# Kernel tuning notes

Hardware: AMD Instinct MI355X
Metric: run time of the kernel (lower is better)

The kernel has to match this reference:

```python
import jax, jax.numpy as jnp
import numpy as np

B, L = 4, 2048
D_MODEL, D_STATE, D_CONV, N_BLOCKS = 128, 16, 8, 6
EXPAND = 2
D_INNER = EXPAND * D_MODEL          # 256
DT_RANK = (D_MODEL + 15) // 16      # 8
CONV_K = 7                          # pre_conv kernel


def setup_inputs() -> dict:
    key = jax.random.key(0)
    ks = jax.random.split(key, 10)
    f = lambda k, s: jax.random.normal(k, s, jnp.float32)
    sc = 0.02
    A_init = jnp.broadcast_to(
        jnp.log(jnp.arange(1, D_STATE + 1, dtype=jnp.float32)),
        (N_BLOCKS, D_INNER, D_STATE)) + 0.0
    return {
        "x": f(ks[0], (B, L, 1)),
        "pre_conv_w": f(ks[1], (D_MODEL, 1, CONV_K)) * sc,
        "pre_conv_b": jnp.zeros((D_MODEL,), jnp.float32),
        "ln_w": jnp.ones((N_BLOCKS, D_MODEL), jnp.float32),
        "ln_b": jnp.zeros((N_BLOCKS, D_MODEL), jnp.float32),
        "W_in": f(ks[2], (N_BLOCKS, 2 * D_INNER, D_MODEL)) * sc,
        "conv_w": f(ks[3], (N_BLOCKS, D_INNER, 1, D_CONV)) * sc,  # depthwise OIH
        "conv_b": jnp.zeros((N_BLOCKS, D_INNER), jnp.float32),
        "W_x": f(ks[4], (N_BLOCKS, DT_RANK + 2 * D_STATE, D_INNER)) * sc,
        "W_dt": f(ks[5], (N_BLOCKS, D_INNER, DT_RANK)) * sc,
        "b_dt": jnp.full((N_BLOCKS, D_INNER), -4.6, jnp.float32),  # softplus ~ 0.01
        "A_log": A_init,
        "D_skip": jnp.ones((N_BLOCKS, D_INNER), jnp.float32),
        "W_out": f(ks[6], (N_BLOCKS, D_MODEL, D_INNER)) * sc,
        "out_w": f(ks[7], (1, D_MODEL)) * sc,
        "out_b": jnp.zeros((1,), jnp.float32),
    }


def _layernorm(x, w, b, eps=1e-5):
    m = jnp.mean(x, axis=-1, keepdims=True)
    v = jnp.mean(jnp.square(x - m), axis=-1, keepdims=True)
    return (x - m) * jax.lax.rsqrt(v + eps) * w + b


def _mamba(x, W_in, cw, cb, W_x, W_dt, b_dt, A_log, D_skip, W_out):
    # x: (B, L, D_MODEL)
    xz = jnp.einsum('bld,ed->ble', x, W_in)            # (B,L,2E)
    xi, z = jnp.split(xz, 2, axis=-1)
    # depthwise causal conv over time
    xc = jax.lax.conv_general_dilated(
        xi.transpose(0, 2, 1), cw, window_strides=(1,),
        padding=[(D_CONV - 1, 0)],
        dimension_numbers=('NCH', 'OIH', 'NCH'),
        feature_group_count=D_INNER) + cb[None, :, None]
    xc = jax.nn.silu(xc).transpose(0, 2, 1)            # (B,L,E)
    dbl = jnp.einsum('ble,re->blr', xc, W_x)
    dt = dbl[..., :DT_RANK]
    Bm = dbl[..., DT_RANK:DT_RANK + D_STATE]           # (B,L,N)
    Cm = dbl[..., DT_RANK + D_STATE:]                  # (B,L,N)
    delta = jax.nn.softplus(jnp.einsum('blr,er->ble', dt, W_dt) + b_dt)
    A = -jnp.exp(A_log)                                # (E,N)

    def step(h, inp):
        d, b, c, u = inp                               # (B,E),(B,N),(B,N),(B,E)
        h = h * jnp.exp(d[..., None] * A) + (d * u)[..., None] * b[:, None, :]
        return h, jnp.einsum('ben,bn->be', h, c)

    h0 = jnp.zeros((x.shape[0], D_INNER, D_STATE), x.dtype)
    xs = (delta.transpose(1, 0, 2), Bm.transpose(1, 0, 2),
          Cm.transpose(1, 0, 2), xc.transpose(1, 0, 2))
    _, ys = jax.lax.scan(step, h0, xs)                 # ys: (L,B,E)
    y = ys.transpose(1, 0, 2) + D_skip * xc
    y = y * jax.nn.silu(z)
    return jnp.einsum('ble,de->bld', y, W_out)


def reference(x, pre_conv_w, pre_conv_b, ln_w, ln_b, W_in, conv_w, conv_b,
              W_x, W_dt, b_dt, A_log, D_skip, W_out, out_w, out_b):
    # pre_conv (1 -> d_model), SAME padding, then exact GELU
    h = jax.lax.conv_general_dilated(
        x.transpose(0, 2, 1), pre_conv_w, window_strides=(1,),
        padding=[(CONV_K // 2, CONV_K // 2)],
        dimension_numbers=('NCH', 'OIH', 'NCH')) + pre_conv_b[None, :, None]
    h = jax.nn.gelu(h, approximate=False).transpose(0, 2, 1)  # (B,L,D)

    def block(carry, p):
        lw, lb, Wi, cw, cb, Wx, Wdt, bdt, Alog, Dsk, Wo = p
        y = _mamba(_layernorm(carry, lw, lb), Wi, cw, cb, Wx, Wdt, bdt, Alog, Dsk, Wo)
        return carry + y, None                         # dropout is identity (eval)

    h, _ = jax.lax.scan(block, h, (ln_w, ln_b, W_in, conv_w, conv_b,
                                   W_x, W_dt, b_dt, A_log, D_skip, W_out))
    return (jnp.einsum('bld,od->blo', h, out_w) + out_b)[..., 0]  # (B,L)
```

## Files before the change

### kernel.cpp

```cpp
#include <hip/hip_runtime.h>
#include <hip/hip_bf16.h>
#include <hip/hip_cooperative_groups.h>
#include <math.h>

namespace cg = cooperative_groups;

#define BB 4
#define LL 2048
#define DM 128
#define DI 256
#define DS 16
#define DTR 8
#define NB 6
#define KPRE 7
#define KC 8
#define NC 128
#define CT 16
#define NCHUNK (BB*NC)
#define BL (BB*LL)
#define SU 4

typedef __attribute__((ext_vector_type(8))) short short8v;
typedef __attribute__((ext_vector_type(4))) short short4v;
typedef __attribute__((ext_vector_type(4))) float f32x4;

__device__ __forceinline__ void store_bf16x4(__hip_bfloat16* p, float a, float b, float c, float d) {
    __hip_bfloat16 t[4] = {__float2bfloat16(a), __float2bfloat16(b),
                           __float2bfloat16(c), __float2bfloat16(d)};
    *(short4v*)p = *(const short4v*)t;
}
__device__ __forceinline__ float4 load_bf16x4(const __hip_bfloat16* p) {
    short4v raw = *(const short4v*)p;
    const __hip_bfloat16* t = (const __hip_bfloat16*)&raw;
    return make_float4(__bfloat162float(t[0]), __bfloat162float(t[1]),
                       __bfloat162float(t[2]), __bfloat162float(t[3]));
}


__device__ __forceinline__ void dev_preconv(int idx,
    const float* __restrict__ x, const float* __restrict__ w, const float* __restrict__ bias,
    float* __restrict__ h, const float* __restrict__ Wi, const float* __restrict__ Wo,
    __hip_bfloat16* __restrict__ wi, __hip_bfloat16* __restrict__ wo) {
    int d = idx & (DM - 1);
    int l = (idx >> 7) & (LL - 1);
    int b = idx >> 18;
    float acc = bias[d];
#pragma unroll
    for (int k = 0; k < KPRE; ++k) {
        int pos = l + k - 3;
        float xv = (pos >= 0 && pos < LL) ? x[b * LL + pos] : 0.f;
        acc = fmaf(xv, w[d * KPRE + k], acc);
    }
    h[idx] = 0.5f * acc * (1.f + erff(acc * 0.70710678118654752f));
    if (idx < NB * 2 * DI * DM) wi[idx] = __float2bfloat16(Wi[idx]);
    if (idx < NB * DM * DI)     wo[idx] = __float2bfloat16(Wo[idx]);
}

__device__ __forceinline__ void dev_ln_gemm1(int v, int wave, int lane,
    const float* __restrict__ h, const float* __restrict__ lw, const float* __restrict__ lb,
    const __hip_bfloat16* __restrict__ W, float* __restrict__ xz,
    __hip_bfloat16* As) {
    int tileM = v >> 2, tileN = v & 3;
    int mBase = tileM * 64, nBase = tileN * 128;
    for (int it = 0; it < 16; ++it) {
        int row = wave * 16 + it;
        int t = mBase + row;
        float v0 = h[t * DM + lane];
        float v1 = h[t * DM + lane + 64];
        float s = v0 + v1;
#pragma unroll
        for (int off = 32; off; off >>= 1) s += __shfl_xor(s, off);
        float mean = s * (1.f / 128.f);
        float d0 = v0 - mean, d1 = v1 - mean;
        float q = d0 * d0 + d1 * d1;
#pragma unroll
        for (int off = 32; off; off >>= 1) q += __shfl_xor(q, off);
        float rstd = rsqrtf(q * (1.f / 128.f) + 1e-5f);
        int sw = (row & 7) << 3;
        As[row * 128 + (lane ^ sw)]        = __float2bfloat16(d0 * rstd * lw[lane] + lb[lane]);
        As[row * 128 + ((lane + 64) ^ sw)] = __float2bfloat16(d1 * rstd * lw[lane + 64] + lb[lane + 64]);
    }
    __syncthreads();
    int r  = lane & 15;
    int kh = lane >> 4;
    f32x4 acc[4][2] = {};
    for (int k0 = 0; k0 < DM; k0 += 32) {
        short8v af[4], bf[2];
#pragma unroll
        for (int i = 0; i < 4; ++i) {
            int row = i * 16 + r;
            int cbk = (k0 >> 3) + kh;
            af[i] = *(const short8v*)&As[row * 128 + ((cbk ^ (row & 7)) << 3)];
        }
#pragma unroll
        for (int j = 0; j < 2; ++j)
            bf[j] = *(const short8v*)&W[(size_t)(nBase + wave * 32 + j * 16 + r) * DM + k0 + kh * 8];
#pragma unroll
        for (int i = 0; i < 4; ++i)
#pragma unroll
            for (int j = 0; j < 2; ++j)
                acc[i][j] = __builtin_amdgcn_mfma_f32_16x16x32_bf16(af[i], bf[j], acc[i][j], 0, 0, 0);
    }
#pragma unroll
    for (int i = 0; i < 4; ++i)
#pragma unroll
        for (int j = 0; j < 2; ++j)
#pragma unroll
            for (int rg = 0; rg < 4; ++rg) {
                size_t off = (size_t)(mBase + i * 16 + kh * 4 + rg) * (2 * DI)
                           + nBase + wave * 32 + j * 16 + r;
                xz[off] = acc[i][j][rg];
            }
    __syncthreads();
}

__device__ __forceinline__ void dev_fusedA(int chunk, int tid,
    const float* __restrict__ xz, const float* __restrict__ cw, const float* __restrict__ cbs,
    const float* __restrict__ Wx, const float* __restrict__ Wdt, const float* __restrict__ bdt,
    const float* __restrict__ A_log,
    __hip_bfloat16* __restrict__ P, __hip_bfloat16* __restrict__ hend,
    float (*xc_s)[DI], float (*dl_s)[DI], float (*bc_s)[32]) {
    int c = chunk & (NC - 1);
    int b = chunk >> 7;
    int wave = tid >> 6, lane = tid & 63;
    for (int i = 0; i < 4; ++i) {
        int lt = wave * 4 + i;
        int tl = c * CT + lt;
        float xv[4];
        for (int j = 0; j < 4; ++j) {
            int e = lane + 64 * j;
            float4 c0 = *(const float4*)&cw[e * KC];
            float4 c1 = *(const float4*)&cw[e * KC + 4];
            float wts[8] = {c0.x, c0.y, c0.z, c0.w, c1.x, c1.y, c1.z, c1.w};
            float acc = cbs[e];
#pragma unroll
            for (int k = 0; k < KC; ++k) {
                int pos = tl + k - (KC - 1);
                float v = (pos >= 0) ? xz[((size_t)(b * LL + pos) << 9) + e] : 0.f;
                acc = fmaf(v, wts[k], acc);
            }
            xv[j] = acc / (1.f + __expf(-acc));
            xc_s[lt][e] = xv[j];
        }
        float dt8[8];
        float bcv = 0.f;
#pragma unroll
        for (int o = 0; o < 40; ++o) {
            const float* w = &Wx[o * DI];
            float s = xv[0] * w[lane];
            s = fmaf(xv[1], w[lane + 64], s);
            s = fmaf(xv[2], w[lane + 128], s);
            s = fmaf(xv[3], w[lane + 192], s);
#pragma unroll
            for (int off = 32; off; off >>= 1) s += __shfl_xor(s, off);
            if (o < 8) dt8[o] = s;
            else if (lane == o - 8) bcv = s;
        }
        if (lane < 32) bc_s[lt][lane] = bcv;
        for (int j = 0; j < 4; ++j) {
            int e = lane + 64 * j;
            float s = bdt[e];
#pragma unroll
            for (int r = 0; r < 8; ++r) s = fmaf(dt8[r], Wdt[e * 8 + r], s);
            dl_s[lt][e] = fmaxf(s, 0.f) + log1pf(__expf(-fabsf(s)));
        }
    }
    __syncthreads();
    int e = tid;
    float d16[CT], u16[CT];
#pragma unroll
    for (int l = 0; l < CT; ++l) { d16[l] = dl_s[l][e]; u16[l] = xc_s[l][e]; }
    for (int ng = 0; ng < 4; ++ng) {
        float4 al = *(const float4*)&A_log[e * DS + 4 * ng];
        float Aen[4] = {-__expf(al.x), -__expf(al.y), -__expf(al.z), -__expf(al.w)};
        float hh[4] = {}, Pl[4] = {1.f, 1.f, 1.f, 1.f};
#pragma unroll
        for (int l = 0; l < CT; ++l) {
            float du = d16[l] * u16[l];
            float4 bm = *(const float4*)&bc_s[l][4 * ng];
            float a0 = __expf(d16[l] * Aen[0]);
            float a1 = __expf(d16[l] * Aen[1]);
            float a2 = __expf(d16[l] * Aen[2]);
            float a3 = __expf(d16[l] * Aen[3]);
            hh[0] = fmaf(hh[0], a0, du * bm.x);
            hh[1] = fmaf(hh[1], a1, du * bm.y);
            hh[2] = fmaf(hh[2], a2, du * bm.z);
            hh[3] = fmaf(hh[3], a3, du * bm.w);
            Pl[0] *= a0; Pl[1] *= a1; Pl[2] *= a2; Pl[3] *= a3;
        }
        size_t oidx = (((size_t)(b * NC + c)) * DI + e) * DS + 4 * ng;
        store_bf16x4(&P[oidx], Pl[0], Pl[1], Pl[2], Pl[3]);
        store_bf16x4(&hend[oidx], hh[0], hh[1], hh[2], hh[3]);
    }
}

__device__ __forceinline__ void dev_carry(int gtid,
    const __hip_bfloat16* __restrict__ P, const __hip_bfloat16* __restrict__ hend,
    __hip_bfloat16* __restrict__ hin) {
    int n = gtid & 15;
    int e = (gtid >> 4) & 255;
    int b = gtid >> 12;
    const size_t cs = (size_t)DI * DS;
    size_t idx0 = (((size_t)(b * NC)) * DI + e) * DS + n;
    float carry = 0.f;
    for (int c0 = 0; c0 < NC; c0 += 8) {
        float p[8], he[8];
#pragma unroll
        for (int j = 0; j < 8; ++j) {
            size_t idx = idx0 + (size_t)(c0 + j) * cs;
            p[j]  = __bfloat162float(P[idx]);
            he[j] = __bfloat162float(hend[idx]);
        }
#pragma unroll
        for (int j = 0; j < 8; ++j) {
            hin[idx0 + (size_t)(c0 + j) * cs] = __float2bfloat16(carry);
            carry = fmaf(p[j], carry, he[j]);
        }
    }
}

__device__ __forceinline__ void dev_fusedB(int chunk, int tid,
    const float* __restrict__ A_log, const __hip_bfloat16* __restrict__ hin,
    const float* __restrict__ xz, const float* __restrict__ Dsk,
    const __hip_bfloat16* __restrict__ Wo, float* __restrict__ hout,
    const float (*xc_s)[DI], const float (*dl_s)[DI], const float (*bc_s)[32],
    __hip_bfloat16 (*y_s)[DI + 8]) {
    int c = chunk & (NC - 1);
    int b = chunk >> 7;
    int base = b * LL + c * CT;
    int e = tid;
    float d16[CT], u16[CT], yacc[CT];
    float dsk = Dsk[e];
#pragma unroll
    for (int l = 0; l < CT; ++l) {
        d16[l] = dl_s[l][e];
        u16[l] = xc_s[l][e];
        yacc[l] = dsk * u16[l];
    }
    for (int ng = 0; ng < 4; ++ng) {
        float4 al = *(const float4*)&A_log[e * DS + 4 * ng];
        float Aen[4] = {-__expf(al.x), -__expf(al.y), -__expf(al.z), -__expf(al.w)};
        float4 h4 = load_bf16x4(&hin[(((size_t)(b * NC + c)) * DI + e) * DS + 4 * ng]);
        float hh[4] = {h4.x, h4.y, h4.z, h4.w};
#pragma unroll
        for (int l = 0; l < CT; ++l) {
            float du = d16[l] * u16[l];
            float4 bm = *(const float4*)&bc_s[l][4 * ng];
            float4 cm = *(const float4*)&bc_s[l][16 + 4 * ng];
            float a0 = __expf(d16[l] * Aen[0]);
            float a1 = __expf(d16[l] * Aen[1]);
            float a2 = __expf(d16[l] * Aen[2]);
            float a3 = __expf(d16[l] * Aen[3]);
            hh[0] = fmaf(hh[0], a0, du * bm.x);
            hh[1] = fmaf(hh[1], a1, du * bm.y);
            hh[2] = fmaf(hh[2], a2, du * bm.z);
            hh[3] = fmaf(hh[3], a3, du * bm.w);
            float p = hh[0] * cm.x;
            p = fmaf(hh[1], cm.y, p);
            p = fmaf(hh[2], cm.z, p);
            p = fmaf(hh[3], cm.w, p);
            yacc[l] += p;
        }
    }
#pragma unroll
    for (int l = 0; l < CT; ++l) {
        float z = xz[((size_t)(base + l) << 9) + DI + e];
        y_s[l][e] = __float2bfloat16(yacc[l] * (z / (1.f + __expf(-z))));
    }
    __syncthreads();
    int wave = tid >> 6, lane = tid & 63;
    int r  = lane & 15;
    int kh = lane >> 4;
    f32x4 acc[2] = {};
    for (int k0 = 0; k0 < DI; k0 += 32) {
        short8v af = *(const short8v*)&y_s[r][k0 + kh * 8];
        short8v bf[2];
#pragma unroll
        for (int j = 0; j < 2; ++j)
            bf[j] = *(const short8v*)&Wo[(size_t)(wave * 32 + j * 16 + r) * DI + k0 + kh * 8];
#pragma unroll
        for (int j = 0; j < 2; ++j)
            acc[j] = __builtin_amdgcn_mfma_f32_16x16x32_bf16(af, bf[j], acc[j], 0, 0, 0);
    }
    __syncthreads();
#pragma unroll
    for (int j = 0; j < 2; ++j)
#pragma unroll
        for (int rg = 0; rg < 4; ++rg) {
            size_t off = (size_t)(base + kh * 4 + rg) * DM + wave * 32 + j * 16 + r;
            hout[off] += acc[j][rg];
        }
}

__device__ __forceinline__ void dev_out(int t, int lane,
    const float* __restrict__ h, const float* __restrict__ ow, const float* __restrict__ ob,
    float* __restrict__ out) {
    float s = h[t * DM + lane] * ow[lane] + h[t * DM + lane + 64] * ow[lane + 64];
#pragma unroll
    for (int off = 32; off; off >>= 1) s += __shfl_xor(s, off);
    if (lane == 0) out[t] = s + ob[0];
}


__device__ __forceinline__ void dev_conv_wx(int t, int lane,
    const float* __restrict__ xz, const float* __restrict__ cw, const float* __restrict__ cbs,
    const float* __restrict__ Wx, const float* __restrict__ Wdt, const float* __restrict__ bdt,
    float* __restrict__ xc, float* __restrict__ BC, float* __restrict__ delta) {
    int tl = t & (LL - 1);
    int b = t >> 11;
    float xv[4];
#pragma unroll
    for (int j = 0; j < 4; ++j) {
        int e = lane + 64 * j;
        float4 cw0 = *(const float4*)&cw[e * KC];
        float4 cw1 = *(const float4*)&cw[e * KC + 4];
        float wts[8] = {cw0.x, cw0.y, cw0.z, cw0.w, cw1.x, cw1.y, cw1.z, cw1.w};
        float acc = cbs[e];
#pragma unroll
        for (int k = 0; k < KC; ++k) {
            int pos = tl + k - (KC - 1);
            float v = (pos >= 0) ? xz[((size_t)(b * LL + pos) << 9) + e] : 0.f;
            acc = fmaf(v, wts[k], acc);
        }
        xv[j] = acc / (1.f + __expf(-acc));
        xc[((size_t)t << 8) + e] = xv[j];
    }
    float dt[8];
    float bcv = 0.f;
#pragma unroll
    for (int o = 0; o < 40; ++o) {
        const float* w = &Wx[o * DI];
        float s = xv[0] * w[lane];
        s = fmaf(xv[1], w[lane + 64], s);
        s = fmaf(xv[2], w[lane + 128], s);
        s = fmaf(xv[3], w[lane + 192], s);
#pragma unroll
        for (int off = 32; off; off >>= 1) s += __shfl_xor(s, off);
        if (o < 8) dt[o] = s;
        else if (lane == o - 8) bcv = s;
    }
    if (lane < 32) BC[((size_t)t << 5) + lane] = bcv;
#pragma unroll
    for (int j = 0; j < 4; ++j) {
        int e = lane + 64 * j;
        float s = bdt[e];
#pragma unroll
        for (int r = 0; r < 8; ++r) s = fmaf(dt[r], Wdt[e * 8 + r], s);
        delta[((size_t)t << 8) + e] = fmaxf(s, 0.f) + log1pf(__expf(-fabsf(s)));
    }
}

__device__ __forceinline__ void dev_scan1(int blk, int tid,
    const float* __restrict__ delta, const float* __restrict__ xc, const float* __restrict__ BC,
    const float* __restrict__ A_log,
    __hip_bfloat16* __restrict__ P, __hip_bfloat16* __restrict__ hend) {
    int eg = blk & 3;
    int c = (blk >> 2) & (NC - 1);
    int b = blk >> 9;
    int e = eg * 64 + (tid >> 2);
    int ng = tid & 3;
    float4 al = *(const float4*)&A_log[e * DS + 4 * ng];
    float Aen[4] = {-__expf(al.x), -__expf(al.y), -__expf(al.z), -__expf(al.w)};
    float h[4] = {}, Pl[4] = {1.f, 1.f, 1.f, 1.f};
    int base = b * LL + c * CT;
    const float* dp = delta + (size_t)base * DI + e;
    const float* up = xc + (size_t)base * DI + e;
    const float* bp = BC + (size_t)base * 32 + 4 * ng;
    for (int l0 = 0; l0 < CT; l0 += SU) {
        float d[SU], u[SU];
        float4 bm[SU];
#pragma unroll
        for (int j = 0; j < SU; ++j) {
            d[j]  = dp[(l0 + j) * DI];
            u[j]  = up[(l0 + j) * DI];
            bm[j] = *(const float4*)&bp[(l0 + j) * 32];
        }
#pragma unroll
        for (int j = 0; j < SU; ++j) {
            float du = d[j] * u[j];
            float a0 = __expf(d[j] * Aen[0]);
            float a1 = __expf(d[j] * Aen[1]);
            float a2 = __expf(d[j] * Aen[2]);
            float a3 = __expf(d[j] * Aen[3]);
            h[0] = fmaf(h[0], a0, du * bm[j].x);
            h[1] = fmaf(h[1], a1, du * bm[j].y);
            h[2] = fmaf(h[2], a2, du * bm[j].z);
            h[3] = fmaf(h[3], a3, du * bm[j].w);
            Pl[0] *= a0; Pl[1] *= a1; Pl[2] *= a2; Pl[3] *= a3;
        }
    }
    size_t oidx = (((size_t)(b * NC + c)) * DI + e) * DS + 4 * ng;
    store_bf16x4(&P[oidx], Pl[0], Pl[1], Pl[2], Pl[3]);
    store_bf16x4(&hend[oidx], h[0], h[1], h[2], h[3]);
}

__device__ __forceinline__ void dev_scan3(int blk, int tid,
    const float* __restrict__ delta, const float* __restrict__ xc, const float* __restrict__ BC,
    const float* __restrict__ A_log, const __hip_bfloat16* __restrict__ hin,
    const float* __restrict__ xz,
    const float* __restrict__ Dsk, __hip_bfloat16* __restrict__ y) {
    int eg = blk & 3;
    int c = (blk >> 2) & (NC - 1);
    int b = blk >> 9;
    int e = eg * 64 + (tid >> 2);
    int ng = tid & 3;
    float4 al = *(const float4*)&A_log[e * DS + 4 * ng];
    float Aen[4] = {-__expf(al.x), -__expf(al.y), -__expf(al.z), -__expf(al.w)};
    float dsk = Dsk[e];
    float4 h4 = load_bf16x4(&hin[(((size_t)(b * NC + c)) * DI + e) * DS + 4 * ng]);
    float h[4] = {h4.x, h4.y, h4.z, h4.w};
    int base = b * LL + c * CT;
    const float* dp = delta + (size_t)base * DI + e;
    const float* up = xc + (size_t)base * DI + e;
    const float* bp = BC + (size_t)base * 32 + 4 * ng;
    const float* zp = xz + ((size_t)base << 9) + DI + e;
    __hip_bfloat16* yp = y + (size_t)base * DI + e;
    for (int l0 = 0; l0 < CT; l0 += SU) {
        float d[SU], u[SU], zv[SU];
        float4 bm[SU], cm[SU];
#pragma unroll
        for (int j = 0; j < SU; ++j) {
            d[j]  = dp[(l0 + j) * DI];
            u[j]  = up[(l0 + j) * DI];
            bm[j] = *(const float4*)&bp[(l0 + j) * 32];
            cm[j] = *(const float4*)&bp[(l0 + j) * 32 + 16];
            zv[j] = zp[(size_t)(l0 + j) << 9];
        }
#pragma unroll
        for (int j = 0; j < SU; ++j) {
            float du = d[j] * u[j];
            float a0 = __expf(d[j] * Aen[0]);
            float a1 = __expf(d[j] * Aen[1]);
            float a2 = __expf(d[j] * Aen[2]);
            float a3 = __expf(d[j] * Aen[3]);
            h[0] = fmaf(h[0], a0, du * bm[j].x);
            h[1] = fmaf(h[1], a1, du * bm[j].y);
            h[2] = fmaf(h[2], a2, du * bm[j].z);
            h[3] = fmaf(h[3], a3, du * bm[j].w);
            float yc = h[0] * cm[j].x;
            yc = fmaf(h[1], cm[j].y, yc);
            yc = fmaf(h[2], cm[j].z, yc);
            yc = fmaf(h[3], cm[j].w, yc);
            yc += __shfl_xor(yc, 1);
            yc += __shfl_xor(yc, 2);
            if (ng == 0) {
                float z = zv[j];
                float val = (yc + dsk * u[j]) * (z / (1.f + __expf(-z)));
                yp[(l0 + j) * DI] = __float2bfloat16(val);
            }
        }
    }
}

__device__ __forceinline__ void dev_gemm2(int v, int wave, int lane,
    const __hip_bfloat16* __restrict__ A, const __hip_bfloat16* __restrict__ W,
    float* __restrict__ C) {
    int mBase = v * 16;
    int r  = lane & 15;
    int kh = lane >> 4;
    f32x4 acc[2] = {};
    for (int k0 = 0; k0 < DI; k0 += 32) {
        short8v af = *(const short8v*)&A[(size_t)(mBase + r) * DI + k0 + kh * 8];
        short8v bf[2];
#pragma unroll
        for (int j = 0; j < 2; ++j)
            bf[j] = *(const short8v*)&W[(size_t)(wave * 32 + j * 16 + r) * DI + k0 + kh * 8];
#pragma unroll
        for (int j = 0; j < 2; ++j)
            acc[j] = __builtin_amdgcn_mfma_f32_16x16x32_bf16(af, bf[j], acc[j], 0, 0, 0);
    }
#pragma unroll
    for (int j = 0; j < 2; ++j)
#pragma unroll
        for (int rg = 0; rg < 4; ++rg) {
            size_t off = (size_t)(mBase + kh * 4 + rg) * DM + wave * 32 + j * 16 + r;
            C[off] += acc[j][rg];
        }
}


struct MegaArgs {
    const float *x, *pcw, *pcb, *ln_w, *ln_b, *W_in, *conv_w, *conv_b;
    const float *W_x, *W_dt, *b_dt, *A_log, *D_skip, *W_out, *out_w, *out_b;
    float *h, *xz, *xc, *BC, *delta, *out;
    __hip_bfloat16 *P, *hend, *hin;
    __hip_bfloat16 *y_bf, *wi_bf, *wo_bf;
};

__global__ __launch_bounds__(256, 2) void k_mega(MegaArgs a) {
    __shared__ union {
        __hip_bfloat16 As[64 * 128];
        __hip_bfloat16 y_s[CT][DI + 8];
    } u;
    __shared__ float xc_s[CT][DI];
    __shared__ float dl_s[CT][DI];
    __shared__ float bc_s[CT][32];
    cg::grid_group g = cg::this_grid();
    int bid = blockIdx.x, tid = threadIdx.x;
    int nb = gridDim.x;
    int wave = tid >> 6, lane = tid & 63;

    for (int v = bid; v < (BB * LL * DM) / 256; v += nb)
        dev_preconv(v * 256 + tid, a.x, a.pcw, a.pcb, a.h, a.W_in, a.W_out, a.wi_bf, a.wo_bf);
    g.sync();

    for (int blk = 0; blk < NB; ++blk) {
        for (int v = bid; v < 512; v += nb)
            dev_ln_gemm1(v, wave, lane, a.h, a.ln_w + blk * DM, a.ln_b + blk * DM,
                         a.wi_bf + (size_t)blk * 2 * DI * DM, a.xz, u.As);
        g.sync();
        dev_fusedA(bid, tid, a.xz, a.conv_w + (size_t)blk * DI * KC,
                   a.conv_b + blk * DI, a.W_x + (size_t)blk * 40 * DI,
                   a.W_dt + (size_t)blk * DI * DTR, a.b_dt + blk * DI,
                   a.A_log + (size_t)blk * DI * DS, a.P, a.hend,
                   xc_s, dl_s, bc_s);
        g.sync();
        for (int v = bid; v < (BB * DI * DS) / 256; v += nb)
            dev_carry(v * 256 + tid, a.P, a.hend, a.hin);
        g.sync();
        dev_fusedB(bid, tid, a.A_log + (size_t)blk * DI * DS, a.hin, a.xz,
                   a.D_skip + blk * DI, a.wo_bf + (size_t)blk * DM * DI, a.h,
                   xc_s, dl_s, bc_s, u.y_s);
        g.sync();
    }

    for (int v = bid; v < BL / 4; v += nb)
        dev_out(v * 4 + wave, lane, a.h, a.out_w, a.out_b, a.out);
}


__global__ void w_preconv(const float* x, const float* w, const float* bias, float* h,
                          const float* Wi, const float* Wo,
                          __hip_bfloat16* wi, __hip_bfloat16* wo) {
    dev_preconv(blockIdx.x * 256 + threadIdx.x, x, w, bias, h, Wi, Wo, wi, wo);
}
__global__ __launch_bounds__(256) void w_ln_gemm1(const float* h, const float* lw, const float* lb,
                                                  const __hip_bfloat16* W, float* xz) {
    __shared__ __hip_bfloat16 As[64 * 128];
    dev_ln_gemm1(blockIdx.x, threadIdx.x >> 6, threadIdx.x & 63, h, lw, lb, W, xz, As);
}
__global__ __launch_bounds__(256) void w_conv_wx(const float* xz, const float* cw, const float* cbs,
                                                 const float* Wx, const float* Wdt, const float* bdt,
                                                 float* xc, float* BC, float* delta) {
    dev_conv_wx(blockIdx.x * 4 + (threadIdx.x >> 6), threadIdx.x & 63,
                xz, cw, cbs, Wx, Wdt, bdt, xc, BC, delta);
}
__global__ __launch_bounds__(256) void w_scan1(const float* delta, const float* xc, const float* BC,
                                               const float* A_log,
                                               __hip_bfloat16* P, __hip_bfloat16* hend) {
    dev_scan1(blockIdx.x, threadIdx.x, delta, xc, BC, A_log, P, hend);
}
__global__ void w_carry(const __hip_bfloat16* P, const __hip_bfloat16* hend, __hip_bfloat16* hin) {
    dev_carry(blockIdx.x * 256 + threadIdx.x, P, hend, hin);
}
__global__ __launch_bounds__(256) void w_scan3(const float* delta, const float* xc, const float* BC,
                                               const float* A_log, const __hip_bfloat16* hin,
                                               const float* xz,
                                               const float* Dsk, __hip_bfloat16* y) {
    dev_scan3(blockIdx.x, threadIdx.x, delta, xc, BC, A_log, hin, xz, Dsk, y);
}
__global__ __launch_bounds__(256) void w_gemm2(const __hip_bfloat16* A, const __hip_bfloat16* W,
                                               float* C) {
    dev_gemm2(blockIdx.x, threadIdx.x >> 6, threadIdx.x & 63, A, W, C);
}
__global__ void w_out(const float* h, const float* ow, const float* ob, float* out) {
    dev_out(blockIdx.x * 4 + (threadIdx.x >> 6), threadIdx.x & 63, h, ow, ob, out);
}

extern "C" void kernel_launch(void* const* d_in, const int* in_sizes, int n_in,
                              void* d_out, int out_size, void* d_ws, size_t ws_size,
                              hipStream_t stream) {
    (void)in_sizes; (void)n_in; (void)out_size; (void)ws_size;
    const float* x      = (const float*)d_in[0];
    const float* pcw    = (const float*)d_in[1];
    const float* pcb    = (const float*)d_in[2];
    const float* ln_w   = (const float*)d_in[3];
    const float* ln_b   = (const float*)d_in[4];
    const float* W_in   = (const float*)d_in[5];
    const float* conv_w = (const float*)d_in[6];
    const float* conv_b = (const float*)d_in[7];
    const float* W_x    = (const float*)d_in[8];
    const float* W_dt   = (const float*)d_in[9];
    const float* b_dt   = (const float*)d_in[10];
    const float* A_log  = (const float*)d_in[11];
    const float* D_skip = (const float*)d_in[12];
    const float* W_out  = (const float*)d_in[13];
    const float* out_w  = (const float*)d_in[14];
    const float* out_b  = (const float*)d_in[15];

    const size_t SCAN_N = (size_t)BB * NC * DI * DS;
    float* ws    = (float*)d_ws;
    float* h     = ws;
    float* xz    = h     + (size_t)BL * DM;
    float* xc    = xz    + (size_t)BL * 2 * DI;
    float* BC    = xc    + (size_t)BL * DI;
    float* delta = BC    + (size_t)BL * 2 * DS;
    __hip_bfloat16* P    = (__hip_bfloat16*)(delta + (size_t)BL * DI);
    __hip_bfloat16* hend = P + SCAN_N;
    __hip_bfloat16* hin  = hend + SCAN_N;
    __hip_bfloat16* y_bf  = hin + SCAN_N;
    __hip_bfloat16* wi_bf = y_bf + (size_t)BL * DI;
    __hip_bfloat16* wo_bf = wi_bf + (size_t)NB * 2 * DI * DM;

    int dev = 0;
    (void)hipGetDevice(&dev);
    int coopAttr = 0;
    (void)hipDeviceGetAttribute(&coopAttr, hipDeviceAttributeCooperativeLaunch, dev);
    int numCU = 0;
    (void)hipDeviceGetAttribute(&numCU, hipDeviceAttributeMultiprocessorCount, dev);
    int maxBpCU = 0;
    (void)hipOccupancyMaxActiveBlocksPerMultiprocessor(&maxBpCU, k_mega, 256, 0);
    int grid = maxBpCU * numCU;
    if (grid > NCHUNK) grid = NCHUNK;

    bool launched = false;
    if (coopAttr && grid == NCHUNK) {
        MegaArgs ma = {x, pcw, pcb, ln_w, ln_b, W_in, conv_w, conv_b,
                       W_x, W_dt, b_dt, A_log, D_skip, W_out, out_w, out_b,
                       h, xz, xc, BC, delta, (float*)d_out,
                       P, hend, hin, y_bf, wi_bf, wo_bf};
        void* kp[] = {&ma};
        hipError_t e = hipLaunchCooperativeKernel((void*)k_mega, dim3(grid), dim3(256), kp, 0, stream);
        launched = (e == hipSuccess);
        if (!launched) (void)hipGetLastError();
    }

    if (!launched) {
        w_preconv<<<(BB * LL * DM) / 256, 256, 0, stream>>>(x, pcw, pcb, h, W_in, W_out, wi_bf, wo_bf);
        for (int blk = 0; blk < NB; ++blk) {
            w_ln_gemm1<<<512, 256, 0, stream>>>(
                h, ln_w + blk * DM, ln_b + blk * DM, wi_bf + (size_t)blk * 2 * DI * DM, xz);
            w_conv_wx<<<BL / 4, 256, 0, stream>>>(
                xz, conv_w + (size_t)blk * DI * KC, conv_b + blk * DI,
                W_x + (size_t)blk * 40 * DI, W_dt + (size_t)blk * DI * DTR,
                b_dt + blk * DI, xc, BC, delta);
            w_scan1<<<BB * NC * 4, 256, 0, stream>>>(
                delta, xc, BC, A_log + (size_t)blk * DI * DS, P, hend);
            w_carry<<<(BB * DI * DS) / 256, 256, 0, stream>>>(P, hend, hin);
            w_scan3<<<BB * NC * 4, 256, 0, stream>>>(
                delta, xc, BC, A_log + (size_t)blk * DI * DS, hin, xz, D_skip + blk * DI, y_bf);
            w_gemm2<<<BL / 16, 256, 0, stream>>>(y_bf, wo_bf + (size_t)blk * DM * DI, h);
        }
        w_out<<<BL / 4, 256, 0, stream>>>(h, out_w, out_b, (float*)d_out);
    }
}
```

Before: 561.5 us.

## Fuse LayerNorm+in-projection GEMM into per-chunk scan phase, recompute halo rows

The separate LN+GEMM1 phase and its grid-wide sync are removed from the cooperative megakernel. Each chunk block now computes LayerNorm and the x-half of the in-projection for its 16 timesteps plus 16 halo rows in shared memory, feeding the causal conv directly. Only the z-half is written to global memory, in bf16. This drops one grid barrier per block and the fp32 xz round trip, at the cost of redundant halo GEMM work, larger shared memory and bf16 rounding of the conv inputs and z.

```diff
diff --git a/kernel.cpp b/kernel.cpp
--- a/kernel.cpp
+++ b/kernel.cpp
@@ -56,76 +56,88 @@
     if (idx < NB * DM * DI)     wo[idx] = __float2bfloat16(Wo[idx]);
 }
 
-__device__ __forceinline__ void dev_ln_gemm1(int v, int wave, int lane,
+__device__ __forceinline__ void dev_phaseA(int chunk, int tid,
     const float* __restrict__ h, const float* __restrict__ lw, const float* __restrict__ lb,
-    const __hip_bfloat16* __restrict__ W, float* __restrict__ xz,
-    __hip_bfloat16* As) {
-    int tileM = v >> 2, tileN = v & 3;
-    int mBase = tileM * 64, nBase = tileN * 128;
-    for (int it = 0; it < 16; ++it) {
-        int row = wave * 16 + it;
-        int t = mBase + row;
-        float v0 = h[t * DM + lane];
-        float v1 = h[t * DM + lane + 64];
-        float s = v0 + v1;
-#pragma unroll
-        for (int off = 32; off; off >>= 1) s += __shfl_xor(s, off);
-        float mean = s * (1.f / 128.f);
-        float d0 = v0 - mean, d1 = v1 - mean;
-        float q = d0 * d0 + d1 * d1;
-#pragma unroll
-        for (int off = 32; off; off >>= 1) q += __shfl_xor(q, off);
-        float rstd = rsqrtf(q * (1.f / 128.f) + 1e-5f);
-        int sw = (row & 7) << 3;
-        As[row * 128 + (lane ^ sw)]        = __float2bfloat16(d0 * rstd * lw[lane] + lb[lane]);
-        As[row * 128 + ((lane + 64) ^ sw)] = __float2bfloat16(d1 * rstd * lw[lane + 64] + lb[lane + 64]);
-    }
-    __syncthreads();
-    int r  = lane & 15;
-    int kh = lane >> 4;
-    f32x4 acc[4][2] = {};
-    for (int k0 = 0; k0 < DM; k0 += 32) {
-        short8v af[4], bf[2];
-#pragma unroll
-        for (int i = 0; i < 4; ++i) {
-            int row = i * 16 + r;
-            int cbk = (k0 >> 3) + kh;
-            af[i] = *(const short8v*)&As[row * 128 + ((cbk ^ (row & 7)) << 3)];
-        }
-#pragma unroll
-        for (int j = 0; j < 2; ++j)
-            bf[j] = *(const short8v*)&W[(size_t)(nBase + wave * 32 + j * 16 + r) * DM + k0 + kh * 8];
-#pragma unroll
-        for (int i = 0; i < 4; ++i)
-#pragma unroll
-            for (int j = 0; j < 2; ++j)
-                acc[i][j] = __builtin_amdgcn_mfma_f32_16x16x32_bf16(af[i], bf[j], acc[i][j], 0, 0, 0);
-    }
-#pragma unroll
-    for (int i = 0; i < 4; ++i)
-#pragma unroll
-        for (int j = 0; j < 2; ++j)
-#pragma unroll
-            for (int rg = 0; rg < 4; ++rg) {
-                size_t off = (size_t)(mBase + i * 16 + kh * 4 + rg) * (2 * DI)
-                           + nBase + wave * 32 + j * 16 + r;
-                xz[off] = acc[i][j][rg];
-            }
-    __syncthreads();
-}
-
-__device__ __forceinline__ void dev_fusedA(int chunk, int tid,
-    const float* __restrict__ xz, const float* __restrict__ cw, const float* __restrict__ cbs,
+    const __hip_bfloat16* __restrict__ Wi,
+    const float* __restrict__ cw, const float* __restrict__ cbs,
     const float* __restrict__ Wx, const float* __restrict__ Wdt, const float* __restrict__ bdt,
     const float* __restrict__ A_log,
     __hip_bfloat16* __restrict__ P, __hip_bfloat16* __restrict__ hend,
+    __hip_bfloat16* __restrict__ z_bf,
+    __hip_bfloat16* As, __hip_bfloat16 (*xi_s)[DI],
     float (*xc_s)[DI], float (*dl_s)[DI], float (*bc_s)[32]) {
     int c = chunk & (NC - 1);
     int b = chunk >> 7;
     int wave = tid >> 6, lane = tid & 63;
+    for (int it = 0; it < 8; ++it) {
+        int lr = wave * 8 + it;
+        int tl = c * CT + lr - 16;
+        int sw = (lr & 7) << 3;
+        if (tl >= 0) {
+            int t = b * LL + tl;
+            float v0 = h[t * DM + lane];
+            float v1 = h[t * DM + lane + 64];
+            float s = v0 + v1;
+#pragma unroll
+            for (int off = 32; off; off >>= 1) s += __shfl_xor(s, off);
+            float mean = s * (1.f / 128.f);
+            float d0 = v0 - mean, d1 = v1 - mean;
+            float q = d0 * d0 + d1 * d1;
+#pragma unroll
+            for (int off = 32; off; off >>= 1) q += __shfl_xor(q, off);
+            float rstd = rsqrtf(q * (1.f / 128.f) + 1e-5f);
+            As[lr * 128 + (lane ^ sw)]        = __float2bfloat16(d0 * rstd * lw[lane] + lb[lane]);
+            As[lr * 128 + ((lane + 64) ^ sw)] = __float2bfloat16(d1 * rstd * lw[lane + 64] + lb[lane + 64]);
+        } else {
+            As[lr * 128 + (lane ^ sw)]        = __float2bfloat16(0.f);
+            As[lr * 128 + ((lane + 64) ^ sw)] = __float2bfloat16(0.f);
+        }
+    }
+    __syncthreads();
+    {
+        int r = lane & 15, kh = lane >> 4;
+        short8v af[2][4];
+#pragma unroll
+        for (int mf = 0; mf < 2; ++mf)
+#pragma unroll
+            for (int k = 0; k < 4; ++k) {
+                int row = mf * 16 + r;
+                int cbk = k * 4 + kh;
+                af[mf][k] = *(const short8v*)&As[row * 128 + ((cbk ^ (row & 7)) << 3)];
+            }
+        int nBase = wave * 128;
+        for (int nf = 0; nf < 8; ++nf) {
+            short8v bfr[4];
+#pragma unroll
+            for (int k = 0; k < 4; ++k)
+                bfr[k] = *(const short8v*)&Wi[(size_t)(nBase + nf * 16 + r) * DM + k * 32 + kh * 8];
+            if (wave < 2) {
+                f32x4 acc0 = {}, acc1 = {};
+#pragma unroll
+                for (int k = 0; k < 4; ++k) {
+                    acc0 = __builtin_amdgcn_mfma_f32_16x16x32_bf16(af[0][k], bfr[k], acc0, 0, 0, 0);
+                    acc1 = __builtin_amdgcn_mfma_f32_16x16x32_bf16(af[1][k], bfr[k], acc1, 0, 0, 0);
+                }
+#pragma unroll
+                for (int rg = 0; rg < 4; ++rg) {
+                    xi_s[kh * 4 + rg][nBase + nf * 16 + r]      = __float2bfloat16(acc0[rg]);
+                    xi_s[16 + kh * 4 + rg][nBase + nf * 16 + r] = __float2bfloat16(acc1[rg]);
+                }
+            } else {
+                f32x4 acc1 = {};
+#pragma unroll
+                for (int k = 0; k < 4; ++k)
+                    acc1 = __builtin_amdgcn_mfma_f32_16x16x32_bf16(af[1][k], bfr[k], acc1, 0, 0, 0);
+#pragma unroll
+                for (int rg = 0; rg < 4; ++rg)
+                    z_bf[(size_t)(b * LL + c * CT + kh * 4 + rg) * DI
+                         + (nBase - 256) + nf * 16 + r] = __float2bfloat16(acc1[rg]);
+            }
+        }
+    }
+    __syncthreads();
     for (int i = 0; i < 4; ++i) {
         int lt = wave * 4 + i;
-        int tl = c * CT + lt;
         float xv[4];
         for (int j = 0; j < 4; ++j) {
             int e = lane + 64 * j;
@@ -134,11 +146,8 @@
             float wts[8] = {c0.x, c0.y, c0.z, c0.w, c1.x, c1.y, c1.z, c1.w};
             float acc = cbs[e];
 #pragma unroll
-            for (int k = 0; k < KC; ++k) {
-                int pos = tl + k - (KC - 1);
-                float v = (pos >= 0) ? xz[((size_t)(b * LL + pos) << 9) + e] : 0.f;
-                acc = fmaf(v, wts[k], acc);
-            }
+            for (int k = 0; k < KC; ++k)
+                acc = fmaf(__bfloat162float(xi_s[lt + 9 + k][e]), wts[k], acc);
             xv[j] = acc / (1.f + __expf(-acc));
             xc_s[lt][e] = xv[j];
         }
@@ -221,7 +230,7 @@
 
 __device__ __forceinline__ void dev_fusedB(int chunk, int tid,
     const float* __restrict__ A_log, const __hip_bfloat16* __restrict__ hin,
-    const float* __restrict__ xz, const float* __restrict__ Dsk,
+    const __hip_bfloat16* __restrict__ z_bf, const float* __restrict__ Dsk,
     const __hip_bfloat16* __restrict__ Wo, float* __restrict__ hout,
     const float (*xc_s)[DI], const float (*dl_s)[DI], const float (*bc_s)[32],
     __hip_bfloat16 (*y_s)[DI + 8]) {
@@ -264,7 +273,7 @@
     }
 #pragma unroll
     for (int l = 0; l < CT; ++l) {
-        float z = xz[((size_t)(base + l) << 9) + DI + e];
+        float z = __bfloat162float(z_bf[(size_t)(base + l) * DI + e]);
         y_s[l][e] = __float2bfloat16(yacc[l] * (z / (1.f + __expf(-z))));
     }
     __syncthreads();
@@ -301,6 +310,64 @@
     if (lane == 0) out[t] = s + ob[0];
 }
 
+
+__device__ __forceinline__ void dev_ln_gemm1(int v, int wave, int lane,
+    const float* __restrict__ h, const float* __restrict__ lw, const float* __restrict__ lb,
+    const __hip_bfloat16* __restrict__ W, float* __restrict__ xz,
+    __hip_bfloat16* As) {
+    int tileM = v >> 2, tileN = v & 3;
+    int mBase = tileM * 64, nBase = tileN * 128;
+    for (int it = 0; it < 16; ++it) {
+        int row = wave * 16 + it;
+        int t = mBase + row;
+        float v0 = h[t * DM + lane];
+        float v1 = h[t * DM + lane + 64];
+        float s = v0 + v1;
+#pragma unroll
+        for (int off = 32; off; off >>= 1) s += __shfl_xor(s, off);
+        float mean = s * (1.f / 128.f);
+        float d0 = v0 - mean, d1 = v1 - mean;
+        float q = d0 * d0 + d1 * d1;
+#pragma unroll
+        for (int off = 32; off; off >>= 1) q += __shfl_xor(q, off);
+        float rstd = rsqrtf(q * (1.f / 128.f) + 1e-5f);
+        int sw = (row & 7) << 3;
+        As[row * 128 + (lane ^ sw)]        = __float2bfloat16(d0 * rstd * lw[lane] + lb[lane]);
+        As[row * 128 + ((lane + 64) ^ sw)] = __float2bfloat16(d1 * rstd * lw[lane + 64] + lb[lane + 64]);
+    }
+    __syncthreads();
+    int r  = lane & 15;
+    int kh = lane >> 4;
+    f32x4 acc[4][2] = {};
+    for (int k0 = 0; k0 < DM; k0 += 32) {
+        short8v af[4], bf[2];
+#pragma unroll
+        for (int i = 0; i < 4; ++i) {
+            int row = i * 16 + r;
+            int cbk = (k0 >> 3) + kh;
+            af[i] = *(const short8v*)&As[row * 128 + ((cbk ^ (row & 7)) << 3)];
+        }
+#pragma unroll
+        for (int j = 0; j < 2; ++j)
+            bf[j] = *(const short8v*)&W[(size_t)(nBase + wave * 32 + j * 16 + r) * DM + k0 + kh * 8];
+#pragma unroll
+        for (int i = 0; i < 4; ++i)
+#pragma unroll
+            for (int j = 0; j < 2; ++j)
+                acc[i][j] = __builtin_amdgcn_mfma_f32_16x16x32_bf16(af[i], bf[j], acc[i][j], 0, 0, 0);
+    }
+#pragma unroll
+    for (int i = 0; i < 4; ++i)
+#pragma unroll
+        for (int j = 0; j < 2; ++j)
+#pragma unroll
+            for (int rg = 0; rg < 4; ++rg) {
+                size_t off = (size_t)(mBase + i * 16 + kh * 4 + rg) * (2 * DI)
+                           + nBase + wave * 32 + j * 16 + r;
+                xz[off] = acc[i][j][rg];
+            }
+    __syncthreads();
+}
 
 __device__ __forceinline__ void dev_conv_wx(int t, int lane,
     const float* __restrict__ xz, const float* __restrict__ cw, const float* __restrict__ cbs,
@@ -480,16 +547,18 @@
 
 
 struct MegaArgs {
-    const float *x, *pcw, *pcb, *ln_w, *ln_b, *W_in, *conv_w, *conv_b;
-    const float *W_x, *W_dt, *b_dt, *A_log, *D_skip, *W_out, *out_w, *out_b;
-    float *h, *xz, *xc, *BC, *delta, *out;
-    __hip_bfloat16 *P, *hend, *hin;
-    __hip_bfloat16 *y_bf, *wi_bf, *wo_bf;
+    const float *x, *pcw, *pcb, *ln_w, *ln_b, *conv_w, *conv_b;
+    const float *W_x, *W_dt, *b_dt, *A_log, *D_skip, *W_in, *W_out, *out_w, *out_b;
+    float *h, *out;
+    __hip_bfloat16 *P, *hend, *hin, *z_bf, *wi_bf, *wo_bf;
 };
 
 __global__ __launch_bounds__(256, 2) void k_mega(MegaArgs a) {
     __shared__ union {
-        __hip_bfloat16 As[64 * 128];
+        struct {
+            __hip_bfloat16 As[32 * 128];
+            __hip_bfloat16 xi[32][DI];
+        } pa;
         __hip_bfloat16 y_s[CT][DI + 8];
     } u;
     __shared__ float xc_s[CT][DI];
@@ -505,20 +574,17 @@
     g.sync();
 
     for (int blk = 0; blk < NB; ++blk) {
-        for (int v = bid; v < 512; v += nb)
-            dev_ln_gemm1(v, wave, lane, a.h, a.ln_w + blk * DM, a.ln_b + blk * DM,
-                         a.wi_bf + (size_t)blk * 2 * DI * DM, a.xz, u.As);
-        g.sync();
-        dev_fusedA(bid, tid, a.xz, a.conv_w + (size_t)blk * DI * KC,
-                   a.conv_b + blk * DI, a.W_x + (size_t)blk * 40 * DI,
-                   a.W_dt + (size_t)blk * DI * DTR, a.b_dt + blk * DI,
-                   a.A_log + (size_t)blk * DI * DS, a.P, a.hend,
-                   xc_s, dl_s, bc_s);
+        dev_phaseA(bid, tid, a.h, a.ln_w + blk * DM, a.ln_b + blk * DM,
+                   a.wi_bf + (size_t)blk * 2 * DI * DM,
+                   a.conv_w + (size_t)blk * DI * KC, a.conv_b + blk * DI,
+                   a.W_x + (size_t)blk * 40 * DI, a.W_dt + (size_t)blk * DI * DTR,
+                   a.b_dt + blk * DI, a.A_log + (size_t)blk * DI * DS,
+                   a.P, a.hend, a.z_bf, u.pa.As, u.pa.xi, xc_s, dl_s, bc_s);
         g.sync();
         for (int v = bid; v < (BB * DI * DS) / 256; v += nb)
             dev_carry(v * 256 + tid, a.P, a.hend, a.hin);
         g.sync();
-        dev_fusedB(bid, tid, a.A_log + (size_t)blk * DI * DS, a.hin, a.xz,
+        dev_fusedB(bid, tid, a.A_log + (size_t)blk * DI * DS, a.hin, a.z_bf,
                    a.D_skip + blk * DI, a.wo_bf + (size_t)blk * DM * DI, a.h,
                    xc_s, dl_s, bc_s, u.y_s);
         g.sync();
@@ -599,7 +665,8 @@
     __hip_bfloat16* hend = P + SCAN_N;
     __hip_bfloat16* hin  = hend + SCAN_N;
     __hip_bfloat16* y_bf  = hin + SCAN_N;
-    __hip_bfloat16* wi_bf = y_bf + (size_t)BL * DI;
+    __hip_bfloat16* z_bf  = y_bf + (size_t)BL * DI;
+    __hip_bfloat16* wi_bf = z_bf + (size_t)BL * DI;
     __hip_bfloat16* wo_bf = wi_bf + (size_t)NB * 2 * DI * DM;
 
     int dev = 0;
@@ -615,10 +682,10 @@
 
     bool launched = false;
     if (coopAttr && grid == NCHUNK) {
-        MegaArgs ma = {x, pcw, pcb, ln_w, ln_b, W_in, conv_w, conv_b,
-                       W_x, W_dt, b_dt, A_log, D_skip, W_out, out_w, out_b,
-                       h, xz, xc, BC, delta, (float*)d_out,
-                       P, hend, hin, y_bf, wi_bf, wo_bf};
+        MegaArgs ma = {x, pcw, pcb, ln_w, ln_b, conv_w, conv_b,
+                       W_x, W_dt, b_dt, A_log, D_skip, W_in, W_out, out_w, out_b,
+                       h, (float*)d_out,
+                       P, hend, hin, z_bf, wi_bf, wo_bf};
         void* kp[] = {&ma};
         hipError_t e = hipLaunchCooperativeKernel((void*)k_mega, dim3(grid), dim3(256), kp, 0, stream);
         launched = (e == hipSuccess);
```

After: 562.0 us. About the same (+0.1%).
